# Optimization experiments

Measured on AMD Instinct MI355X. Metric: run time of the kernel, lower is better.

The kernel has to match this reference:

```python
import jax, jax.numpy as jnp
import numpy as np

N = 100000
E = 1600000
IN_C = 128
OUT_C = 64
ALPHA = 0.2  # LeakyReLU negative slope


def _xavier(key, shape, gain=1.414):
    fan_in, fan_out = shape[-2] if len(shape) > 1 else shape[-1], shape[-1]
    bound = gain * np.sqrt(6.0 / (shape[0] * 0 + (shape[-2] if len(shape) > 1 else 1) + shape[-1])) if False else gain * np.sqrt(6.0 / (sum(shape)))
    return jax.random.uniform(key, shape, jnp.float32, -bound, bound)


def setup_inputs() -> dict:
    key = jax.random.key(0)
    k_x, k_s, k_o, k_w, k_a = jax.random.split(key, 5)
    x = jax.random.normal(k_x, (N, IN_C), jnp.float32)
    # edge list with no self-loops (so remove_self_loops is a no-op)
    src = jax.random.randint(k_s, (E,), 0, N)
    off = jax.random.randint(k_o, (E,), 1, N)
    dst = (src + off) % N
    edge_index = jnp.stack([src, dst]).astype(jnp.int64)
    W = _xavier(k_w, (IN_C, OUT_C))
    a = _xavier(k_a, (1, 2 * OUT_C))
    return {"x": x, "W": W, "a": a, "edge_index": edge_index}


def reference(x, W, a, edge_index):
    h = x @ W                               # [N, D]
    n, d = h.shape
    loops = jnp.arange(n, dtype=edge_index.dtype)
    src = jnp.concatenate([edge_index[0], loops])   # add_self_loops
    dst = jnp.concatenate([edge_index[1], loops])
    # (cat(h[src], h[dst]) * a).sum(-1) == h[src]@a1 + h[dst]@a2
    a1, a2 = a[0, :d], a[0, d:]
    s = h @ a1                              # [N]
    t = h @ a2                              # [N]
    edge_e = jnp.exp(jax.nn.leaky_relu(s[src] + t[dst], negative_slope=ALPHA))  # [E+N]
    e_expsum = jax.ops.segment_sum(edge_e, src, num_segments=n)                  # [N]
    h_prime = jax.ops.segment_sum(edge_e[:, None] * h[dst], src, num_segments=n)  # [N, D]
    return h_prime / e_expsum[:, None]
```

## Files before the change

### kernel.cpp

```cpp
#include <hip/hip_runtime.h>
#include <math.h>

#define IN_C 128
#define OUT_C 64
#define ALPHA 0.2f

#define LDK 136

#define BSH 7
#define NPB 128
#define MAXB 1024
#define PA_EPT 32
#define PA_TILE (256 * PA_EPT)
#define CHUNK 4096

typedef __attribute__((ext_vector_type(8))) short short8;
typedef __attribute__((ext_vector_type(4))) float v4f;

__device__ __forceinline__ ushort f2b(float f) {
  unsigned u = __float_as_uint(f);
  u += 0x7fffu + ((u >> 16) & 1u);
  return (ushort)(u >> 16);
}

__global__ __launch_bounds__(256) void gemm_st_kernel(
    const float* __restrict__ x, const float* __restrict__ W,
    const float* __restrict__ a, ushort* __restrict__ hb,
    float* __restrict__ s, float* __restrict__ t, int* __restrict__ gcur,
    int nbuck, int cape, int n_nodes, int n_tiles) {
  __shared__ ushort xs[64 * LDK];
  __shared__ ushort ws[64 * LDK];

  const int tid = threadIdx.x;
  const int wave = tid >> 6;
  const int lane = tid & 63;
  const int li = lane & 15;
  const int quad = lane >> 4;

  if (blockIdx.x == 0) {
    for (int i = tid; i < nbuck; i += 256) gcur[i] = i * cape;
  }

  for (int i = tid; i < IN_C * OUT_C; i += 256) {
    const int k = i >> 6;
    const int n = i & 63;
    ws[n * LDK + k] = f2b(W[i]);
  }
  __syncthreads();

  short8 bfrag[4][4];
#pragma unroll
  for (int ct = 0; ct < 4; ++ct)
#pragma unroll
    for (int kk = 0; kk < 4; ++kk)
      bfrag[ct][kk] =
          *(const short8*)&ws[(ct * 16 + li) * LDK + kk * 32 + quad * 8];

  float a1v[4], a2v[4];
#pragma unroll
  for (int ct = 0; ct < 4; ++ct) {
    a1v[ct] = a[ct * 16 + li];
    a2v[ct] = a[OUT_C + ct * 16 + li];
  }

  for (int tile = blockIdx.x; tile < n_tiles; tile += gridDim.x) {
    const int row0 = tile * 64;

    __syncthreads();
    for (int i = tid; i < 64 * (IN_C / 4); i += 256) {
      const int r = i >> 5;
      const int c4 = i & 31;
      int row = row0 + r;
      row = row < n_nodes ? row : n_nodes - 1;
      const float4 v = *(const float4*)&x[(size_t)row * IN_C + c4 * 4];
      uint2 p;
      p.x = (unsigned)f2b(v.x) | ((unsigned)f2b(v.y) << 16);
      p.y = (unsigned)f2b(v.z) | ((unsigned)f2b(v.w) << 16);
      *(uint2*)&xs[r * LDK + c4 * 4] = p;
    }
    __syncthreads();

    v4f acc[4];
#pragma unroll
    for (int ct = 0; ct < 4; ++ct) acc[ct] = (v4f){0.f, 0.f, 0.f, 0.f};

    const int rbase = wave * 16;
#pragma unroll
    for (int kk = 0; kk < 4; ++kk) {
      const short8 af =
          *(const short8*)&xs[(rbase + li) * LDK + kk * 32 + quad * 8];
#pragma unroll
      for (int ct = 0; ct < 4; ++ct)
        acc[ct] = __builtin_amdgcn_mfma_f32_16x16x32_bf16(af, bfrag[ct][kk],
                                                          acc[ct], 0, 0, 0);
    }

    const int growbase = row0 + rbase + quad * 4;
    float ps[4] = {0.f, 0.f, 0.f, 0.f};
    float pt[4] = {0.f, 0.f, 0.f, 0.f};
#pragma unroll
    for (int ct = 0; ct < 4; ++ct) {
#pragma unroll
      for (int r = 0; r < 4; ++r) {
        const float hv = acc[ct][r];
        ps[r] += hv * a1v[ct];
        pt[r] += hv * a2v[ct];
        const int grow = growbase + r;
        if (grow < n_nodes)
          hb[(size_t)grow * OUT_C + ct * 16 + li] = f2b(hv);
      }
    }
#pragma unroll
    for (int m = 1; m <= 8; m <<= 1) {
#pragma unroll
      for (int r = 0; r < 4; ++r) {
        ps[r] += __shfl_xor(ps[r], m, 64);
        pt[r] += __shfl_xor(pt[r], m, 64);
      }
    }
    if (li < 4) {
      const int grow = growbase + li;
      if (grow < n_nodes) {
        const float sv = li == 0 ? ps[0] : li == 1 ? ps[1] : li == 2 ? ps[2] : ps[3];
        const float tv = li == 0 ? pt[0] : li == 1 ? pt[1] : li == 2 ? pt[2] : pt[3];
        s[grow] = sv;
        t[grow] = tv;
      }
    }
  }
}

__global__ __launch_bounds__(256) void pa_bin(
    const int* __restrict__ src, const int* __restrict__ dst,
    const float* __restrict__ s, const float* __restrict__ t,
    int* __restrict__ gcur, int2* __restrict__ pairs, int nbuck, int cape,
    int E) {
  __shared__ int hist[MAXB];
  __shared__ int cur[MAXB];
  const int tid = threadIdx.x;
  for (int i = tid; i < nbuck; i += 256) hist[i] = 0;
  __syncthreads();

  const int e0 = blockIdx.x * PA_TILE + tid * PA_EPT;
  if (e0 + PA_EPT <= E) {
#pragma unroll
    for (int i = 0; i < PA_EPT / 4; ++i) {
      const int4 v = *(const int4*)(src + e0 + i * 4);
      atomicAdd(&hist[v.x >> BSH], 1);
      atomicAdd(&hist[v.y >> BSH], 1);
      atomicAdd(&hist[v.z >> BSH], 1);
      atomicAdd(&hist[v.w >> BSH], 1);
    }
  } else {
    for (int e = e0; e < E; ++e) atomicAdd(&hist[src[e] >> BSH], 1);
  }
  __syncthreads();

  for (int i = tid; i < nbuck; i += 256) {
    const int c = hist[i];
    cur[i] = c ? atomicAdd(&gcur[i], c) : 0;
  }
  __syncthreads();

#define EMIT(sv, dv)                                                       \
  {                                                                        \
    const int bkt = (sv) >> BSH;                                           \
    const float z = s[sv] + t[dv];                                         \
    const float w = expf(z > 0.f ? z : ALPHA * z);                         \
    const int pos = atomicAdd(&cur[bkt], 1);                               \
    if (pos < (bkt + 1) * cape)                                            \
      pairs[pos] =                                                         \
          make_int2((((sv) & (NPB - 1)) << 25) | (dv), __float_as_int(w)); \
  }

  if (e0 + PA_EPT <= E) {
#pragma unroll
    for (int i = 0; i < PA_EPT / 4; ++i) {
      const int4 sv = *(const int4*)(src + e0 + i * 4);
      const int4 dv = *(const int4*)(dst + e0 + i * 4);
      EMIT(sv.x, dv.x);
      EMIT(sv.y, dv.y);
      EMIT(sv.z, dv.z);
      EMIT(sv.w, dv.w);
    }
  } else {
    for (int e = e0; e < E; ++e) {
      const int sv = src[e];
      const int dv = dst[e];
      EMIT(sv, dv);
    }
  }
#undef EMIT
}

#define ACC8(o, p, wgt)                                      \
  acc[(o) + 0] += (wgt)*__uint_as_float((p).x << 16);        \
  acc[(o) + 1] += (wgt)*__uint_as_float((p).x & 0xffff0000u);\
  acc[(o) + 2] += (wgt)*__uint_as_float((p).y << 16);        \
  acc[(o) + 3] += (wgt)*__uint_as_float((p).y & 0xffff0000u);\
  acc[(o) + 4] += (wgt)*__uint_as_float((p).z << 16);        \
  acc[(o) + 5] += (wgt)*__uint_as_float((p).z & 0xffff0000u);\
  acc[(o) + 6] += (wgt)*__uint_as_float((p).w << 16);        \
  acc[(o) + 7] += (wgt)*__uint_as_float((p).w & 0xffff0000u);

__global__ __launch_bounds__(256) void aggregate_sorted(
    const int2* __restrict__ pairs, const int* __restrict__ gcur,
    const uint4* __restrict__ hb4, const float* __restrict__ s,
    const float* __restrict__ t, float* __restrict__ out, int n_nodes,
    int cape) {
  __shared__ int2 sl[CHUNK];
  __shared__ int cnt[NPB];
  __shared__ int loffs[NPB];
  __shared__ int cur[NPB];
  __shared__ int w0tot_sh;

  const int b = blockIdx.x;
  const int tid = threadIdx.x;
  const int base = b * cape;
  int fill = gcur[b] - base;
  fill = fill < cape ? fill : cape;

  const int local = tid >> 1;
  const int half = tid & 1;

  float acc[32];
#pragma unroll
  for (int i = 0; i < 32; ++i) acc[i] = 0.f;
  float den = 0.f;

  for (int c0 = 0; c0 < fill; c0 += CHUNK) {
    const int clen = min(CHUNK, fill - c0);
    if (tid < NPB) cnt[tid] = 0;
    __syncthreads();

    int2 pw[CHUNK / 256];
#pragma unroll
    for (int j = 0; j < CHUNK / 256; ++j) {
      const int k = j * 256 + tid;
      if (k < clen) {
        pw[j] = pairs[base + c0 + k];
        atomicAdd(&cnt[((unsigned)pw[j].x) >> 25], 1);
      }
    }
    __syncthreads();

    int c = 0, incl = 0;
    if (tid < NPB) {
      c = cnt[tid];
      incl = c;
#pragma unroll
      for (int off = 1; off < 64; off <<= 1) {
        const int o = __shfl_up(incl, off, 64);
        if ((tid & 63) >= off) incl += o;
      }
      if (tid == 63) w0tot_sh = incl;
    }
    __syncthreads();
    if (tid < NPB) {
      if (tid >= 64) incl += w0tot_sh;
      loffs[tid] = incl - c;
      cur[tid] = incl - c;
    }
    __syncthreads();

#pragma unroll
    for (int j = 0; j < CHUNK / 256; ++j) {
      const int k = j * 256 + tid;
      if (k < clen) {
        const int lo = ((unsigned)pw[j].x) >> 25;
        const int pos = atomicAdd(&cur[lo], 1);
        sl[pos] = make_int2(pw[j].x & 0x1ffffff, pw[j].y);
      }
    }
    __syncthreads();

    const int s0 = loffs[local];
    const int s1 = s0 + cnt[local];
    int e = s0;
    for (; e + 1 < s1; e += 2) {
      const int2 ea = sl[e];
      const int2 eb = sl[e + 1];
      const uint4* ra = &hb4[(size_t)ea.x * 8 + half * 4];
      const uint4* rb = &hb4[(size_t)eb.x * 8 + half * 4];
      const uint4 pa0 = ra[0], pa1 = ra[1], pa2 = ra[2], pa3 = ra[3];
      const uint4 pb0 = rb[0], pb1 = rb[1], pb2 = rb[2], pb3 = rb[3];
      const float wa = __int_as_float(ea.y);
      const float wb = __int_as_float(eb.y);
      ACC8(0, pa0, wa) ACC8(8, pa1, wa) ACC8(16, pa2, wa) ACC8(24, pa3, wa)
      ACC8(0, pb0, wb) ACC8(8, pb1, wb) ACC8(16, pb2, wb) ACC8(24, pb3, wb)
      den += wa + wb;
    }
    if (e < s1) {
      const int2 ea = sl[e];
      const uint4* ra = &hb4[(size_t)ea.x * 8 + half * 4];
      const uint4 pa0 = ra[0], pa1 = ra[1], pa2 = ra[2], pa3 = ra[3];
      const float wa = __int_as_float(ea.y);
      ACC8(0, pa0, wa) ACC8(8, pa1, wa) ACC8(16, pa2, wa) ACC8(24, pa3, wa)
      den += wa;
    }
    __syncthreads();
  }

  const int u = b * NPB + local;
  if (u < n_nodes) {
    const float z0 = s[u] + t[u];
    const float w0 = expf(z0 > 0.f ? z0 : ALPHA * z0);
    const uint4* rs = &hb4[(size_t)u * 8 + half * 4];
    const uint4 q0 = rs[0], q1 = rs[1], q2 = rs[2], q3 = rs[3];
    ACC8(0, q0, w0) ACC8(8, q1, w0) ACC8(16, q2, w0) ACC8(24, q3, w0)
    den += w0;
    const float inv = 1.f / den;
#pragma unroll
    for (int q = 0; q < 8; ++q) {
      float4 o;
      o.x = acc[q * 4 + 0] * inv;
      o.y = acc[q * 4 + 1] * inv;
      o.z = acc[q * 4 + 2] * inv;
      o.w = acc[q * 4 + 3] * inv;
      *(float4*)&out[(size_t)u * OUT_C + half * 32 + q * 4] = o;
    }
  }
}

extern "C" void kernel_launch(void* const* d_in, const int* in_sizes, int n_in,
                              void* d_out, int out_size, void* d_ws,
                              size_t ws_size, hipStream_t stream) {
  const float* x = (const float*)d_in[0];
  const float* W = (const float*)d_in[1];
  const float* a = (const float*)d_in[2];
  const int* edge_index = (const int*)d_in[3];

  const int n_nodes = in_sizes[0] / IN_C;
  const int E = in_sizes[3] / 2;
  const int* src = edge_index;
  const int* dst = edge_index + E;

  float* out = (float*)d_out;

  const int nbuck = (n_nodes + NPB - 1) >> BSH;
  const int cape = (((E + nbuck - 1) / nbuck) + 768 + 15) & ~15;
  const int nblk_bin = (E + PA_TILE - 1) / PA_TILE;

  ushort* hb = (ushort*)d_ws;
  float* s = (float*)(hb + (size_t)n_nodes * OUT_C);
  float* t = s + n_nodes;
  int* gcur = (int*)(t + n_nodes);
  int2* pairs = (int2*)(gcur + MAXB);

  {
    const int n_tiles = (n_nodes + 63) / 64;
    gemm_st_kernel<<<n_tiles, 256, 0, stream>>>(x, W, a, hb, s, t, gcur, nbuck,
                                                cape, n_nodes, n_tiles);
  }

  pa_bin<<<nblk_bin, 256, 0, stream>>>(src, dst, s, t, gcur, pairs, nbuck,
                                       cape, E);

  aggregate_sorted<<<nbuck, 256, 0, stream>>>(pairs, gcur, (const uint4*)hb, s,
                                              t, out, n_nodes, cape);
}
```

Baseline: 197.8 us.

## Retune binning block shape, unroll aggregation by four, cap GEMM grid

After: 202.7 us. +2.5%, slower.

```diff
diff --git a/kernel.cpp b/kernel.cpp
--- a/kernel.cpp
+++ b/kernel.cpp
@@ -10,8 +10,9 @@
 #define BSH 7
 #define NPB 128
 #define MAXB 1024
-#define PA_EPT 32
-#define PA_TILE (256 * PA_EPT)
+#define PA_EPT 4
+#define PA_THREADS 1024
+#define PA_TILE (PA_THREADS * PA_EPT)
 #define CHUNK 4096
 
 typedef __attribute__((ext_vector_type(8))) short short8;
@@ -130,7 +131,7 @@
   }
 }
 
-__global__ __launch_bounds__(256) void pa_bin(
+__global__ __launch_bounds__(PA_THREADS) void pa_bin(
     const int* __restrict__ src, const int* __restrict__ dst,
     const float* __restrict__ s, const float* __restrict__ t,
     int* __restrict__ gcur, int2* __restrict__ pairs, int nbuck, int cape,
@@ -138,25 +139,22 @@
   __shared__ int hist[MAXB];
   __shared__ int cur[MAXB];
   const int tid = threadIdx.x;
-  for (int i = tid; i < nbuck; i += 256) hist[i] = 0;
+  for (int i = tid; i < nbuck; i += PA_THREADS) hist[i] = 0;
   __syncthreads();
 
   const int e0 = blockIdx.x * PA_TILE + tid * PA_EPT;
   if (e0 + PA_EPT <= E) {
-#pragma unroll
-    for (int i = 0; i < PA_EPT / 4; ++i) {
-      const int4 v = *(const int4*)(src + e0 + i * 4);
-      atomicAdd(&hist[v.x >> BSH], 1);
-      atomicAdd(&hist[v.y >> BSH], 1);
-      atomicAdd(&hist[v.z >> BSH], 1);
-      atomicAdd(&hist[v.w >> BSH], 1);
-    }
+    const int4 v = *(const int4*)(src + e0);
+    atomicAdd(&hist[v.x >> BSH], 1);
+    atomicAdd(&hist[v.y >> BSH], 1);
+    atomicAdd(&hist[v.z >> BSH], 1);
+    atomicAdd(&hist[v.w >> BSH], 1);
   } else {
     for (int e = e0; e < E; ++e) atomicAdd(&hist[src[e] >> BSH], 1);
   }
   __syncthreads();
 
-  for (int i = tid; i < nbuck; i += 256) {
+  for (int i = tid; i < nbuck; i += PA_THREADS) {
     const int c = hist[i];
     cur[i] = c ? atomicAdd(&gcur[i], c) : 0;
   }
@@ -174,15 +172,12 @@
   }
 
   if (e0 + PA_EPT <= E) {
-#pragma unroll
-    for (int i = 0; i < PA_EPT / 4; ++i) {
-      const int4 sv = *(const int4*)(src + e0 + i * 4);
-      const int4 dv = *(const int4*)(dst + e0 + i * 4);
-      EMIT(sv.x, dv.x);
-      EMIT(sv.y, dv.y);
-      EMIT(sv.z, dv.z);
-      EMIT(sv.w, dv.w);
-    }
+    const int4 sv = *(const int4*)(src + e0);
+    const int4 dv = *(const int4*)(dst + e0);
+    EMIT(sv.x, dv.x);
+    EMIT(sv.y, dv.y);
+    EMIT(sv.z, dv.z);
+    EMIT(sv.w, dv.w);
   } else {
     for (int e = e0; e < E; ++e) {
       const int sv = src[e];
@@ -277,20 +272,30 @@
     const int s0 = loffs[local];
     const int s1 = s0 + cnt[local];
     int e = s0;
-    for (; e + 1 < s1; e += 2) {
+    for (; e + 3 < s1; e += 4) {
       const int2 ea = sl[e];
       const int2 eb = sl[e + 1];
+      const int2 ec = sl[e + 2];
+      const int2 ed = sl[e + 3];
       const uint4* ra = &hb4[(size_t)ea.x * 8 + half * 4];
       const uint4* rb = &hb4[(size_t)eb.x * 8 + half * 4];
+      const uint4* rc = &hb4[(size_t)ec.x * 8 + half * 4];
+      const uint4* rd = &hb4[(size_t)ed.x * 8 + half * 4];
       const uint4 pa0 = ra[0], pa1 = ra[1], pa2 = ra[2], pa3 = ra[3];
       const uint4 pb0 = rb[0], pb1 = rb[1], pb2 = rb[2], pb3 = rb[3];
+      const uint4 pc0 = rc[0], pc1 = rc[1], pc2 = rc[2], pc3 = rc[3];
+      const uint4 pd0 = rd[0], pd1 = rd[1], pd2 = rd[2], pd3 = rd[3];
       const float wa = __int_as_float(ea.y);
       const float wb = __int_as_float(eb.y);
+      const float wc = __int_as_float(ec.y);
+      const float wd = __int_as_float(ed.y);
       ACC8(0, pa0, wa) ACC8(8, pa1, wa) ACC8(16, pa2, wa) ACC8(24, pa3, wa)
       ACC8(0, pb0, wb) ACC8(8, pb1, wb) ACC8(16, pb2, wb) ACC8(24, pb3, wb)
-      den += wa + wb;
-    }
-    if (e < s1) {
+      ACC8(0, pc0, wc) ACC8(8, pc1, wc) ACC8(16, pc2, wc) ACC8(24, pc3, wc)
+      ACC8(0, pd0, wd) ACC8(8, pd1, wd) ACC8(16, pd2, wd) ACC8(24, pd3, wd)
+      den += (wa + wb) + (wc + wd);
+    }
+    for (; e < s1; ++e) {
       const int2 ea = sl[e];
       const uint4* ra = &hb4[(size_t)ea.x * 8 + half * 4];
       const uint4 pa0 = ra[0], pa1 = ra[1], pa2 = ra[2], pa3 = ra[3];
@@ -349,12 +354,13 @@
 
   {
     const int n_tiles = (n_nodes + 63) / 64;
-    gemm_st_kernel<<<n_tiles, 256, 0, stream>>>(x, W, a, hb, s, t, gcur, nbuck,
-                                                cape, n_nodes, n_tiles);
-  }
-
-  pa_bin<<<nblk_bin, 256, 0, stream>>>(src, dst, s, t, gcur, pairs, nbuck,
-                                       cape, E);
+    const int ngrid = n_tiles < 512 ? n_tiles : 512;
+    gemm_st_kernel<<<ngrid, 256, 0, stream>>>(x, W, a, hb, s, t, gcur, nbuck,
+                                              cape, n_nodes, n_tiles);
+  }
+
+  pa_bin<<<nblk_bin, PA_THREADS, 0, stream>>>(src, dst, s, t, gcur, pairs,
+                                              nbuck, cape, E);
 
   aggregate_sorted<<<nbuck, 256, 0, stream>>>(pairs, gcur, (const uint4*)hb, s,
                                               t, out, n_nodes, cape);
```
